# Performance work log

Hardware: AMD Instinct MI355X
Metric: run time of the kernel (lower is better)

The kernel has to match this reference:

```python
import jax, jax.numpy as jnp
import numpy as np

N_NODES = 50000
N_EDGES = 600000
D_IN = 128
D_HID = 128
D_OUT = 64


def setup_inputs() -> dict:
    key = jax.random.key(0)
    ks = jax.random.split(key, 8)
    x = jax.random.normal(ks[0], (N_NODES, D_IN), dtype=jnp.float32)
    edge_index = jax.random.randint(ks[1], (2, N_EDGES), 0, N_NODES, dtype=jnp.int32)
    s = 0.05
    W1l = jax.random.normal(ks[2], (D_HID, D_IN), dtype=jnp.float32) * s
    b1 = jnp.zeros((D_HID,), dtype=jnp.float32)
    W1r = jax.random.normal(ks[3], (D_HID, D_IN), dtype=jnp.float32) * s
    W2l = jax.random.normal(ks[4], (D_OUT, D_HID), dtype=jnp.float32) * s
    b2 = jnp.zeros((D_OUT,), dtype=jnp.float32)
    W2r = jax.random.normal(ks[5], (D_OUT, D_HID), dtype=jnp.float32) * s
    return {"x": x, "edge_index": edge_index, "W1l": W1l, "b1": b1,
            "W1r": W1r, "W2l": W2l, "b2": b2, "W2r": W2r}


def _sage_conv(x, src, dst, Wl, bl, Wr, n_nodes):
    # mean aggregation of source features at destination nodes
    msg_sum = jax.ops.segment_sum(x[src], dst, num_segments=n_nodes)  # [N, D]
    deg = jax.ops.segment_sum(jnp.ones((src.shape[0], 1), x.dtype), dst,
                              num_segments=n_nodes)                   # [N, 1]
    mean = msg_sum / jnp.maximum(deg, 1.0)
    # out = lin_l(mean_neighbors) + lin_r(x_self); bias only on lin_l (PyG default)
    return mean @ Wl.T + bl + x @ Wr.T


def reference(x, edge_index, W1l, b1, W1r, W2l, b2, W2r):
    src, dst = edge_index[0], edge_index[1]
    n = x.shape[0]
    h = jax.nn.relu(_sage_conv(x, src, dst, W1l, b1, W1r, n))
    # dropout p=0.5 is identity in eval mode (training=False)
    return _sage_conv(h, src, dst, W2l, b2, W2r, n)
```

## Files before the change

kernel.cpp:

```cpp
#include <hip/hip_runtime.h>
#include <hip/hip_bf16.h>

typedef __bf16 bf16x8 __attribute__((ext_vector_type(8)));
typedef float f32x4 __attribute__((ext_vector_type(4)));

#define D_FEAT 128
#define CHUNK 1024
#define NW 49344

__device__ __forceinline__ float bits_to_f(unsigned int u) {
    union { unsigned int i; float f; } c; c.i = u; return c.f;
}
__device__ __forceinline__ unsigned short f_to_bf16(float f) {
    __hip_bfloat16 h = (__hip_bfloat16)f;
    return *(unsigned short*)&h;
}
__device__ __forceinline__ float ld(const void* p, int is16, size_t i) {
    return is16 ? (float)((const __hip_bfloat16*)p)[i] : ((const float*)p)[i];
}
__device__ __forceinline__ int wave_probe16(const void* p) {
    const unsigned short v = ((const unsigned short*)p)[(threadIdx.x & 63) * 2];
    int e = (v >> 7) & 0xFF;
    unsigned long long m = __ballot(e >= 100 && e <= 140);
    return (__popcll(m) >= 48) ? 1 : 0;
}

__global__ void setup_kernel(const void* x,
                             const void* W1l, const void* b1, const void* W1r,
                             const void* W2l, const void* b2, const void* W2r,
                             const int* __restrict__ dst, int E,
                             unsigned short* __restrict__ wout, int* __restrict__ deg) {
    int i = blockIdx.x * blockDim.x + threadIdx.x;
    if (i < NW) {
        int is16 = wave_probe16(x);
        const void* s; int base;
        if      (i < 16384) { s = W1l; base = 0; }
        else if (i < 32768) { s = W1r; base = 16384; }
        else if (i < 40960) { s = W2l; base = 32768; }
        else if (i < 49152) { s = W2r; base = 40960; }
        else if (i < 49280) { s = b1;  base = 49152; }
        else                { s = b2;  base = 49280; }
        wout[i] = f_to_bf16(ld(s, is16, i - base));
    } else {
        int j = i - NW;
        if (j < E) atomicAdd(&deg[dst[j]], 1);
    }
}

__global__ void scan1_kernel(const int* __restrict__ deg, int* __restrict__ bsum, int n) {
    __shared__ int ws[4];
    const int lane = threadIdx.x & 63, wv = threadIdx.x >> 6;
    int i0 = blockIdx.x * CHUNK + threadIdx.x * 4;
    int s = 0;
    #pragma unroll
    for (int j = 0; j < 4; ++j)
        if (i0 + j < n) { int d = deg[i0 + j]; s += (d + 3) & ~3; }
    #pragma unroll
    for (int d = 1; d < 64; d <<= 1) s += __shfl_xor(s, d, 64);
    if (lane == 0) ws[wv] = s;
    __syncthreads();
    if (threadIdx.x == 0) bsum[blockIdx.x] = ws[0] + ws[1] + ws[2] + ws[3];
}

__global__ void scan3_kernel(const int* __restrict__ deg, const int* __restrict__ bsum,
                             int nb, int* __restrict__ off, int* __restrict__ cursor,
                             int* __restrict__ esrc, int n) {
    __shared__ int ws[4];
    const int lane = threadIdx.x & 63, wv = threadIdx.x >> 6;
    int bv = (lane < nb) ? bsum[lane] : 0;
    int bsc = bv;
    #pragma unroll
    for (int s = 1; s < 64; s <<= 1) {
        int t = __shfl_up(bsc, s, 64);
        if (lane >= s) bsc += t;
    }
    const int base = __shfl(bsc, blockIdx.x, 64) - __shfl(bv, blockIdx.x, 64);
    const int total = __shfl(bsc, nb - 1, 64);

    int i0 = blockIdx.x * CHUNK + threadIdx.x * 4;
    int d0 = 0, d1 = 0, d2 = 0, d3 = 0;
    if (i0 + 0 < n) d0 = deg[i0 + 0];
    if (i0 + 1 < n) d1 = deg[i0 + 1];
    if (i0 + 2 < n) d2 = deg[i0 + 2];
    if (i0 + 3 < n) d3 = deg[i0 + 3];
    int v0 = (d0 + 3) & ~3, v1 = (d1 + 3) & ~3, v2 = (d2 + 3) & ~3, v3 = (d3 + 3) & ~3;
    int tsum = v0 + v1 + v2 + v3;
    int sc = tsum;
    #pragma unroll
    for (int s = 1; s < 64; s <<= 1) {
        int t = __shfl_up(sc, s, 64);
        if (lane >= s) sc += t;
    }
    if (lane == 63) ws[wv] = sc;
    __syncthreads();
    int woff = 0;
    for (int w = 0; w < wv; ++w) woff += ws[w];
    int p = base + woff + (sc - tsum);
    #define EMIT(idx, dj, vj)                                            \
        if (i0 + idx < n) {                                              \
            off[i0 + idx] = p; cursor[i0 + idx] = p;                     \
            for (int q = p + dj; q < p + vj; ++q) esrc[q] = n;           \
            p += vj;                                                     \
        }
    EMIT(0, d0, v0) EMIT(1, d1, v1) EMIT(2, d2, v2) EMIT(3, d3, v3)
    #undef EMIT
    if (blockIdx.x == 0 && threadIdx.x == 0) off[n] = total;
}

__global__ void fill_kernel(const int* __restrict__ src, const int* __restrict__ dst,
                            int* __restrict__ cursor, int* __restrict__ esrc, int E) {
    int i = blockIdx.x * blockDim.x + threadIdx.x;
    if (i < E) {
        int p = atomicAdd(&cursor[dst[i]], 1);
        esrc[p] = src[i];
    }
}

template <int NOUT, bool PROBE_A>
__global__ __launch_bounds__(256)
void gemm_dual_kernel(const void* __restrict__ A,
                      const unsigned short* __restrict__ Wa,
                      const unsigned short* __restrict__ Wb,
                      const unsigned short* __restrict__ bias,
                      unsigned short* __restrict__ za, unsigned short* __restrict__ zb,
                      unsigned int* __restrict__ zrow, int zrow_words, int N) {
    if (blockIdx.x == 0 && threadIdx.x < zrow_words) zrow[threadIdx.x] = 0;
    int a16 = 1;
    if (PROBE_A) a16 = wave_probe16(A);

    const int lane = threadIdx.x & 63;
    const int wave = threadIdx.x >> 6;
    const int m0 = (blockIdx.x * 4 + wave) * 16;
    if (m0 >= N) return;
    const int lrow = lane & 15;
    const int kg = lane >> 4;
    const int grow = min(m0 + lrow, N - 1);
    constexpr int NT = NOUT / 16;
    f32x4 aL[NT], aR[NT];
    #pragma unroll
    for (int t = 0; t < NT; ++t) { aL[t] = (f32x4){0,0,0,0}; aR[t] = (f32x4){0,0,0,0}; }

    #pragma unroll
    for (int ks = 0; ks < 4; ++ks) {
        const int k0 = ks * 32 + kg * 8;
        bf16x8 a;
        if (a16) {
            a = *(const bf16x8*)((const unsigned short*)A + (size_t)grow * D_FEAT + k0);
        } else {
            const float* fp = (const float*)A + (size_t)grow * D_FEAT + k0;
            float4 f0 = *(const float4*)fp, f1 = *(const float4*)(fp + 4);
            union { bf16x8 v; unsigned short us[8]; } t;
            t.us[0] = f_to_bf16(f0.x); t.us[1] = f_to_bf16(f0.y);
            t.us[2] = f_to_bf16(f0.z); t.us[3] = f_to_bf16(f0.w);
            t.us[4] = f_to_bf16(f1.x); t.us[5] = f_to_bf16(f1.y);
            t.us[6] = f_to_bf16(f1.z); t.us[7] = f_to_bf16(f1.w);
            a = t.v;
        }
        #pragma unroll
        for (int t = 0; t < NT; ++t) {
            bf16x8 bL = *(const bf16x8*)(Wa + (size_t)(t * 16 + lrow) * D_FEAT + k0);
            aL[t] = __builtin_amdgcn_mfma_f32_16x16x32_bf16(a, bL, aL[t], 0, 0, 0);
            bf16x8 bR = *(const bf16x8*)(Wb + (size_t)(t * 16 + lrow) * D_FEAT + k0);
            aR[t] = __builtin_amdgcn_mfma_f32_16x16x32_bf16(a, bR, aR[t], 0, 0, 0);
        }
    }
    const int orow0 = m0 + kg * 4;
    #pragma unroll
    for (int t = 0; t < NT; ++t) {
        const int col = t * 16 + lrow;
        float bv = bits_to_f((unsigned int)bias[col] << 16);
        #pragma unroll
        for (int r = 0; r < 4; ++r) {
            int orow = orow0 + r;
            if (orow < N) {
                za[(size_t)orow * NOUT + col] = f_to_bf16(aL[t][r]);
                zb[(size_t)orow * NOUT + col] = f_to_bf16(aR[t][r] + bv);
            }
        }
    }
}

__global__ __launch_bounds__(256)
void agg1_kernel(const unsigned short* __restrict__ zl,
                 unsigned short* __restrict__ h,
                 const int* __restrict__ off, const int* __restrict__ deg,
                 const int* __restrict__ esrc, int N) {
    const int lane = threadIdx.x & 63;
    const int wave = threadIdx.x >> 6;
    const int a_lo = (blockIdx.x * 4 + wave) * 8;
    if (a_lo >= N) return;
    const int a_hi = min(a_lo + 8, N);
    const int nn = a_hi - a_lo;
    int offv = off[min(a_lo + min(lane, 8), N)];
    int degv = deg[min(a_lo + min(lane, 7), N - 1)];
    #define OFFAT(i) __shfl(offv, (i), 64)
    const int e_beg = OFFAT(0);
    const int e_end = OFFAT(nn);
    const int quarter = lane >> 4;
    const int fl = lane & 15;
    float ax[8];
    #pragma unroll
    for (int i = 0; i < 8; ++i) ax[i] = 0.f;
    int g = a_lo;
    int gend = OFFAT(1);

    auto flush = [&](int gg) {
        int td = __shfl(degv, gg - a_lo, 64);
        float inv = 1.f / (float)(td > 0 ? td : 1);
        float v[8];
        #pragma unroll
        for (int i = 0; i < 8; ++i) {
            float s = ax[i];
            s += __shfl_xor(s, 16, 64); s += __shfl_xor(s, 32, 64);
            v[i] = s * inv; ax[i] = 0.f;
        }
        if (quarter == 0) {
            unsigned short* hp = h + (size_t)gg * D_FEAT + fl * 8;
            uint4 zr = *(const uint4*)hp;
            unsigned int w[4] = {zr.x, zr.y, zr.z, zr.w};
            unsigned int pk[4];
            #pragma unroll
            for (int i = 0; i < 4; ++i) {
                float r0 = fmaxf(v[2 * i]     + bits_to_f(w[i] << 16), 0.f);
                float r1 = fmaxf(v[2 * i + 1] + bits_to_f(w[i] & 0xffff0000u), 0.f);
                pk[i] = (unsigned int)f_to_bf16(r0) | ((unsigned int)f_to_bf16(r1) << 16);
            }
            *(uint4*)hp = make_uint4(pk[0], pk[1], pk[2], pk[3]);
        }
    };

    int cur = (e_beg < e_end) ? esrc[min(e_beg + (lane & 31), e_end - 1)] : 0;
    for (int e = e_beg; e < e_end; e += 32) {
        int nxt = (e + 32 < e_end) ? esrc[min(e + 32 + (lane & 31), e_end - 1)] : 0;
        uint4 r[8];
        #pragma unroll
        for (int k = 0; k < 8; ++k) {
            int sk = __shfl(cur, 4 * k + quarter, 64);
            r[k] = *(const uint4*)(zl + (size_t)sk * D_FEAT + fl * 8);
        }
        #pragma unroll
        for (int k = 0; k < 8; ++k) {
            const int eb = e + 4 * k;
            if (eb < e_end) {
                while (eb >= gend) {
                    flush(g); ++g;
                    gend = OFFAT(min(g - a_lo + 1, 8));
                }
                uint4 u = r[k];
                ax[0] += bits_to_f(u.x << 16); ax[1] += bits_to_f(u.x & 0xffff0000u);
                ax[2] += bits_to_f(u.y << 16); ax[3] += bits_to_f(u.y & 0xffff0000u);
                ax[4] += bits_to_f(u.z << 16); ax[5] += bits_to_f(u.z & 0xffff0000u);
                ax[6] += bits_to_f(u.w << 16); ax[7] += bits_to_f(u.w & 0xffff0000u);
            }
        }
        cur = nxt;
    }
    while (g < a_hi) {
        flush(g); ++g;
        gend = OFFAT(min(g - a_lo + 1, 8));
    }
    #undef OFFAT
}

__global__ __launch_bounds__(256)
void agg2_kernel(const unsigned short* __restrict__ z2l,
                 const unsigned short* __restrict__ s2,
                 void* __restrict__ out, const void* __restrict__ x,
                 const int* __restrict__ off, const int* __restrict__ deg,
                 const int* __restrict__ esrc, int N) {
    const int o16 = wave_probe16(x);
    const int lane = threadIdx.x & 63;
    const int wave = threadIdx.x >> 6;
    const int a_lo = (blockIdx.x * 4 + wave) * 8;
    if (a_lo >= N) return;
    const int a_hi = min(a_lo + 8, N);
    const int nn = a_hi - a_lo;
    int offv = off[min(a_lo + min(lane, 8), N)];
    int degv = deg[min(a_lo + min(lane, 7), N - 1)];
    #define OFFAT(i) __shfl(offv, (i), 64)
    const int e_beg = OFFAT(0);
    const int e_end = OFFAT(nn);
    const int quarter = lane >> 4;
    const int fl = lane & 15;
    float ax[4];
    #pragma unroll
    for (int i = 0; i < 4; ++i) ax[i] = 0.f;
    int g = a_lo;
    int gend = OFFAT(1);

    auto flush = [&](int gg) {
        int td = __shfl(degv, gg - a_lo, 64);
        float inv = 1.f / (float)(td > 0 ? td : 1);
        float v[4];
        #pragma unroll
        for (int i = 0; i < 4; ++i) {
            float s = ax[i];
            s += __shfl_xor(s, 16, 64); s += __shfl_xor(s, 32, 64);
            v[i] = s * inv; ax[i] = 0.f;
        }
        if (quarter == 0) {
            uint2 sb = *(const uint2*)(s2 + (size_t)gg * 64 + fl * 4);
            v[0] += bits_to_f(sb.x << 16); v[1] += bits_to_f(sb.x & 0xffff0000u);
            v[2] += bits_to_f(sb.y << 16); v[3] += bits_to_f(sb.y & 0xffff0000u);
            if (o16) {
                unsigned int p0 = (unsigned int)f_to_bf16(v[0]) | ((unsigned int)f_to_bf16(v[1]) << 16);
                unsigned int p1 = (unsigned int)f_to_bf16(v[2]) | ((unsigned int)f_to_bf16(v[3]) << 16);
                *(uint2*)((unsigned short*)out + (size_t)gg * 64 + fl * 4) = make_uint2(p0, p1);
            } else {
                *(float4*)((float*)out + (size_t)gg * 64 + fl * 4) =
                    make_float4(v[0], v[1], v[2], v[3]);
            }
        }
    };

    int cur = (e_beg < e_end) ? esrc[min(e_beg + (lane & 31), e_end - 1)] : 0;
    for (int e = e_beg; e < e_end; e += 32) {
        int nxt = (e + 32 < e_end) ? esrc[min(e + 32 + (lane & 31), e_end - 1)] : 0;
        uint2 r[8];
        #pragma unroll
        for (int k = 0; k < 8; ++k) {
            int sk = __shfl(cur, 4 * k + quarter, 64);
            r[k] = *(const uint2*)(z2l + (size_t)sk * 64 + fl * 4);
        }
        #pragma unroll
        for (int k = 0; k < 8; ++k) {
            const int eb = e + 4 * k;
            if (eb < e_end) {
                while (eb >= gend) {
                    flush(g); ++g;
                    gend = OFFAT(min(g - a_lo + 1, 8));
                }
                uint2 u = r[k];
                ax[0] += bits_to_f(u.x << 16); ax[1] += bits_to_f(u.x & 0xffff0000u);
                ax[2] += bits_to_f(u.y << 16); ax[3] += bits_to_f(u.y & 0xffff0000u);
            }
        }
        cur = nxt;
    }
    while (g < a_hi) {
        flush(g); ++g;
        gend = OFFAT(min(g - a_lo + 1, 8));
    }
    #undef OFFAT
}

extern "C" void kernel_launch(void* const* d_in, const int* in_sizes, int n_in,
                              void* d_out, int out_size, void* d_ws, size_t ws_size,
                              hipStream_t stream) {
    const void* x   = d_in[0];
    const int* eidx = (const int*)d_in[1];
    const void* W1l = d_in[2];
    const void* b1  = d_in[3];
    const void* W1r = d_in[4];
    const void* W2l = d_in[5];
    const void* b2  = d_in[6];
    const void* W2r = d_in[7];

    const int N = in_sizes[0] / D_FEAT;
    const int E = in_sizes[1] / 2;
    const int* src = eidx;
    const int* dst = eidx + E;

    char* ws = (char*)d_ws;
    size_t o = 0;
    auto alloc = [&](size_t bytes) -> void* {
        void* p = ws + o;
        o += (bytes + 255) & ~(size_t)255;
        return p;
    };
    int* deg    = (int*)alloc((size_t)N * 4);
    int* off    = (int*)alloc((size_t)(N + 1) * 4);
    int* cursor = (int*)alloc((size_t)N * 4);
    int* bsum   = (int*)alloc(64 * 4);
    int* esrc   = (int*)alloc((size_t)(E + 3 * N + 64) * 4);
    unsigned short* wconv = (unsigned short*)alloc(NW * 2);
    unsigned short* zl = (unsigned short*)alloc((size_t)(N + 1) * D_FEAT * 2);
    unsigned short* h  = (unsigned short*)alloc((size_t)N * D_FEAT * 2);
    unsigned short* z2l = zl;
    unsigned short* s2  = zl + (size_t)(N + 1) * 64;
    (void)n_in; (void)out_size; (void)ws_size;

    hipMemsetAsync(deg, 0, (size_t)N * 4, stream);
    setup_kernel<<<(NW + E + 255) / 256, 256, 0, stream>>>(
        x, W1l, b1, W1r, W2l, b2, W2r, dst, E, wconv, deg);
    const int nchunk = (N + CHUNK - 1) / CHUNK;
    scan1_kernel<<<nchunk, 256, 0, stream>>>(deg, bsum, N);
    scan3_kernel<<<nchunk, 256, 0, stream>>>(deg, bsum, nchunk, off, cursor, esrc, N);
    fill_kernel<<<(E + 255) / 256, 256, 0, stream>>>(src, dst, cursor, esrc, E);

    const int gblocks = (N + 63) / 64;
    const int ablocks = (N + 31) / 32;
    gemm_dual_kernel<128, true><<<gblocks, 256, 0, stream>>>(
        x, wconv + 0, wconv + 16384, wconv + 49152,
        zl, h, (unsigned int*)(zl + (size_t)N * D_FEAT), 64, N);
    agg1_kernel<<<ablocks, 256, 0, stream>>>(zl, h, off, deg, esrc, N);
    gemm_dual_kernel<64, false><<<gblocks, 256, 0, stream>>>(
        h, wconv + 32768, wconv + 40960, wconv + 49280,
        z2l, s2, (unsigned int*)(z2l + (size_t)N * 64), 32, N);
    agg2_kernel<<<ablocks, 256, 0, stream>>>(z2l, s2, d_out, x, off, deg, esrc, N);
}
```

Measured before the change: 257.5 us.

## Split dual GEMM across waves and swap MFMA operands for vectorized stores

Each pair of waves now covers 32 rows, and each wave computes only one of the two weight products (left or right) instead of both. Swapping the MFMA operands (weights as A, features as B) transposes the accumulator layout, so each lane holds four consecutive output columns of one row and can write them as one packed 8-byte store. Scalar 2-byte scattered stores go away, and each weight fragment load is reused across two row tiles. The cost is that each input row is loaded by two waves, and register use for the preloaded feature fragments goes up.

```diff
diff --git a/kernel.cpp b/kernel.cpp
--- a/kernel.cpp
+++ b/kernel.cpp
@@ -130,51 +130,71 @@
 
     const int lane = threadIdx.x & 63;
     const int wave = threadIdx.x >> 6;
-    const int m0 = (blockIdx.x * 4 + wave) * 16;
+    const int sel = wave & 1;
+    const int m0 = blockIdx.x * 64 + (wave >> 1) * 32;
     if (m0 >= N) return;
     const int lrow = lane & 15;
     const int kg = lane >> 4;
-    const int grow = min(m0 + lrow, N - 1);
+    const unsigned short* W = sel ? Wb : Wa;
+    unsigned short* z = sel ? zb : za;
     constexpr int NT = NOUT / 16;
-    f32x4 aL[NT], aR[NT];
-    #pragma unroll
-    for (int t = 0; t < NT; ++t) { aL[t] = (f32x4){0,0,0,0}; aR[t] = (f32x4){0,0,0,0}; }
+
+    bf16x8 xf[2][4];
+    #pragma unroll
+    for (int rt = 0; rt < 2; ++rt) {
+        const int gr = min(m0 + rt * 16 + lrow, N - 1);
+        #pragma unroll
+        for (int ks = 0; ks < 4; ++ks) {
+            const int k0 = ks * 32 + kg * 8;
+            if (a16) {
+                xf[rt][ks] = *(const bf16x8*)((const unsigned short*)A + (size_t)gr * D_FEAT + k0);
+            } else {
+                const float* fp = (const float*)A + (size_t)gr * D_FEAT + k0;
+                float4 f0 = *(const float4*)fp, f1 = *(const float4*)(fp + 4);
+                union { bf16x8 v; unsigned short us[8]; } t;
+                t.us[0] = f_to_bf16(f0.x); t.us[1] = f_to_bf16(f0.y);
+                t.us[2] = f_to_bf16(f0.z); t.us[3] = f_to_bf16(f0.w);
+                t.us[4] = f_to_bf16(f1.x); t.us[5] = f_to_bf16(f1.y);
+                t.us[6] = f_to_bf16(f1.z); t.us[7] = f_to_bf16(f1.w);
+                xf[rt][ks] = t.v;
+            }
+        }
+    }
+
+    f32x4 acc[2][NT];
+    #pragma unroll
+    for (int rt = 0; rt < 2; ++rt)
+        #pragma unroll
+        for (int t = 0; t < NT; ++t) acc[rt][t] = (f32x4){0, 0, 0, 0};
 
     #pragma unroll
     for (int ks = 0; ks < 4; ++ks) {
         const int k0 = ks * 32 + kg * 8;
-        bf16x8 a;
-        if (a16) {
-            a = *(const bf16x8*)((const unsigned short*)A + (size_t)grow * D_FEAT + k0);
-        } else {
-            const float* fp = (const float*)A + (size_t)grow * D_FEAT + k0;
-            float4 f0 = *(const float4*)fp, f1 = *(const float4*)(fp + 4);
-            union { bf16x8 v; unsigned short us[8]; } t;
-            t.us[0] = f_to_bf16(f0.x); t.us[1] = f_to_bf16(f0.y);
-            t.us[2] = f_to_bf16(f0.z); t.us[3] = f_to_bf16(f0.w);
-            t.us[4] = f_to_bf16(f1.x); t.us[5] = f_to_bf16(f1.y);
-            t.us[6] = f_to_bf16(f1.z); t.us[7] = f_to_bf16(f1.w);
-            a = t.v;
-        }
         #pragma unroll
         for (int t = 0; t < NT; ++t) {
-            bf16x8 bL = *(const bf16x8*)(Wa + (size_t)(t * 16 + lrow) * D_FEAT + k0);
-            aL[t] = __builtin_amdgcn_mfma_f32_16x16x32_bf16(a, bL, aL[t], 0, 0, 0);
-            bf16x8 bR = *(const bf16x8*)(Wb + (size_t)(t * 16 + lrow) * D_FEAT + k0);
-            aR[t] = __builtin_amdgcn_mfma_f32_16x16x32_bf16(a, bR, aR[t], 0, 0, 0);
-        }
-    }
-    const int orow0 = m0 + kg * 4;
-    #pragma unroll
-    for (int t = 0; t < NT; ++t) {
-        const int col = t * 16 + lrow;
-        float bv = bits_to_f((unsigned int)bias[col] << 16);
-        #pragma unroll
-        for (int r = 0; r < 4; ++r) {
-            int orow = orow0 + r;
-            if (orow < N) {
-                za[(size_t)orow * NOUT + col] = f_to_bf16(aL[t][r]);
-                zb[(size_t)orow * NOUT + col] = f_to_bf16(aR[t][r] + bv);
+            bf16x8 wf = *(const bf16x8*)(W + (size_t)(t * 16 + lrow) * D_FEAT + k0);
+            acc[0][t] = __builtin_amdgcn_mfma_f32_16x16x32_bf16(wf, xf[0][ks], acc[0][t], 0, 0, 0);
+            acc[1][t] = __builtin_amdgcn_mfma_f32_16x16x32_bf16(wf, xf[1][ks], acc[1][t], 0, 0, 0);
+        }
+    }
+
+    #pragma unroll
+    for (int rt = 0; rt < 2; ++rt) {
+        const int nd = m0 + rt * 16 + lrow;
+        if (nd < N) {
+            #pragma unroll
+            for (int t = 0; t < NT; ++t) {
+                const int c0 = t * 16 + kg * 4;
+                float v0 = acc[rt][t][0], v1 = acc[rt][t][1];
+                float v2 = acc[rt][t][2], v3 = acc[rt][t][3];
+                if (sel) {
+                    uint2 bb = *(const uint2*)(bias + c0);
+                    v0 += bits_to_f(bb.x << 16); v1 += bits_to_f(bb.x & 0xffff0000u);
+                    v2 += bits_to_f(bb.y << 16); v3 += bits_to_f(bb.y & 0xffff0000u);
+                }
+                unsigned int p0 = (unsigned int)f_to_bf16(v0) | ((unsigned int)f_to_bf16(v1) << 16);
+                unsigned int p1 = (unsigned int)f_to_bf16(v2) | ((unsigned int)f_to_bf16(v3) << 16);
+                *(uint2*)(z + (size_t)nd * NOUT + c0) = make_uint2(p0, p1);
             }
         }
     }
```

Result: faster. 246.8 us (-4.2%).
